# Optimization experiments

Measured on AMD Instinct MI355X. Metric: run time of the kernel, lower is better.

Reference implementation:

```python
import jax, jax.numpy as jnp
import numpy as np

NUM_SAMPLES = 1024


def _cdist(a, b):
    # a, b: (n, 3) -> (n, n) pairwise euclidean distances (torch.cdist p=2)
    d2 = jnp.sum((a[:, None, :] - b[None, :, :]) ** 2, axis=-1)
    return jnp.sqrt(jnp.maximum(d2, 0.0))


def _greedy_match_cost(cost):
    # Greedy sequential matching: repeatedly take the global argmin over
    # still-unmatched rows/cols, accumulate its cost, eliminate row+col.
    n = cost.shape[0]

    def step(carry, _):
        row_mask, col_mask, loss = carry
        valid = row_mask[:, None] & col_mask[None, :]
        masked = jnp.where(valid, cost, jnp.inf)
        idx = jnp.argmin(masked)  # row-major first-min == torch's min(dim=1)+argmin tiebreak
        r = idx // n
        c = idx % n
        loss = loss + cost[r, c]
        return (row_mask.at[r].set(False), col_mask.at[c].set(False), loss), None

    init = (jnp.ones((n,), dtype=bool), jnp.ones((n,), dtype=bool), jnp.float32(0.0))
    (_, _, loss), _ = jax.lax.scan(step, init, None, length=n)
    return loss / n


def setup_inputs() -> dict:
    key = jax.random.key(0)
    k1, k2, k3 = jax.random.split(key, 3)
    B, N, n = 8, 4096, NUM_SAMPLES
    S1 = jax.random.normal(k1, (B, N, 3), dtype=jnp.float32)
    S2 = jax.random.normal(k2, (B, N, 3), dtype=jnp.float32)
    # torch.randperm(N)[:n] per batch element: without-replacement sampling
    perm_keys = jax.random.split(k3, B)
    indices = jax.vmap(lambda k: jax.random.permutation(k, N)[:n])(perm_keys).astype(jnp.int32)
    return {"S1": S1, "S2": S2, "indices": indices}


def reference(S1, S2, indices):
    # sample the same indices from both sets, per batch (matches original loop)
    s1 = jnp.take_along_axis(S1, indices[:, :, None], axis=1)  # (B, n, 3)
    s2 = jnp.take_along_axis(S2, indices[:, :, None], axis=1)  # (B, n, 3)
    cost = jax.vmap(_cdist)(s1, s2)  # (B, n, n)
    losses = jax.vmap(_greedy_match_cost)(cost)  # (B,)
    return jnp.mean(losses)
```

## Files before the change

kernel.cpp:

```cpp
#include <hip/hip_runtime.h>
#include <stdint.h>

#define BATCH 8
#define NPTS 4096
#define NS 1024
#define KD 6

typedef unsigned long long u64;
typedef unsigned int u32;
typedef unsigned short u16;
typedef unsigned char u8;

#define DEADV (~0ull)
#define QNANB 0x7FC00000u
#define INFB  0x7F800000u

__device__ __forceinline__ float pdist3(float ax, float ay, float az,
                                        float bx, float by, float bz) {
    float dx = ax - bx, dy = ay - by, dz = az - bz;
    float d2 = __fmaf_rn(dz, dz, __fmaf_rn(dy, dy, dx * dx));
    return __fsqrt_rn(d2);
}

__device__ __forceinline__ u64 packv(float d, u32 row, u32 col) {
    return ((u64)__float_as_uint(d) << 20) | ((u64)row << 10) | (u64)col;
}

__device__ __forceinline__ u64 u64min2(u64 a, u64 b) { return a < b ? a : b; }

__device__ __forceinline__ u64 tree16(const u64* p) {
    u64 a0 = u64min2(p[0], p[1]),   a1 = u64min2(p[2], p[3]);
    u64 a2 = u64min2(p[4], p[5]),   a3 = u64min2(p[6], p[7]);
    u64 a4 = u64min2(p[8], p[9]),   a5 = u64min2(p[10], p[11]);
    u64 a6 = u64min2(p[12], p[13]), a7 = u64min2(p[14], p[15]);
    u64 b0 = u64min2(a0, a1), b1 = u64min2(a2, a3);
    u64 b2 = u64min2(a4, a5), b3 = u64min2(a6, a7);
    return u64min2(u64min2(b0, b1), u64min2(b2, b3));
}

template<int CTRL>
__device__ __forceinline__ u64 dpp_min_step(u64 m) {
    u32 lo = (u32)m, hi = (u32)(m >> 32);
    u32 olo = (u32)__builtin_amdgcn_update_dpp(-1, (int)lo, CTRL, 0xF, 0xF, false);
    u32 ohi = (u32)__builtin_amdgcn_update_dpp(-1, (int)hi, CTRL, 0xF, 0xF, false);
    u64 o = ((u64)ohi << 32) | olo;
    return o < m ? o : m;
}

__device__ __forceinline__ u64 wave_min_u64(u64 m) {
    m = dpp_min_step<0x111>(m);
    m = dpp_min_step<0x112>(m);
    m = dpp_min_step<0x114>(m);
    m = dpp_min_step<0x118>(m);
    m = dpp_min_step<0x142>(m);
    m = dpp_min_step<0x143>(m);
    u32 lo = (u32)__builtin_amdgcn_readlane((int)(u32)m, 63);
    u32 hi = (u32)__builtin_amdgcn_readlane((int)(u32)(m >> 32), 63);
    return ((u64)hi << 32) | lo;
}

__global__ void gather_k(const float* __restrict__ S1, const float* __restrict__ S2,
                         const int* __restrict__ idx,
                         float4* __restrict__ s1g, float4* __restrict__ s2g,
                         int* __restrict__ cnt) {
    int t = blockIdx.x * blockDim.x + threadIdx.x;
    if (t == 0) *cnt = 0;
    if (t >= BATCH * NS) return;
    int b = t >> 10;
    int j = idx[t];
    const float* p1 = S1 + ((size_t)b * NPTS + j) * 3;
    const float* p2 = S2 + ((size_t)b * NPTS + j) * 3;
    s1g[t] = make_float4(p1[0], p1[1], p1[2], 0.f);
    s2g[t] = make_float4(p2[0], p2[1], p2[2], 0.f);
}

__global__ void lists_k(const float4* __restrict__ s1g, const float4* __restrict__ s2g,
                        u64* __restrict__ rlist_g, u64* __restrict__ clist_g) {
    __shared__ float4 pts[NS];
    int gg = blockIdx.x * 4 + (threadIdx.x >> 6);
    int lane = threadIdx.x & 63;
    int side = (gg >= BATCH * NS) ? 1 : 0;
    int g = gg - side * (BATCH * NS);
    int b = g >> 10;
    u32 rc = (u32)(g & 1023);
    const float4* other = (side ? s1g : s2g) + (size_t)b * NS;
    for (int i = threadIdx.x; i < NS; i += 256) pts[i] = other[i];
    float4 a = side ? s2g[g] : s1g[g];
    __syncthreads();
    u64 cand[16];
    #pragma unroll
    for (int k = 0; k < 16; ++k) {
        int o = lane + (k << 6);
        float4 q = pts[o];
        float d = pdist3(a.x, a.y, a.z, q.x, q.y, q.z);
        cand[k] = side ? packv(d, (u32)o, rc) : packv(d, rc, (u32)o);
    }
    u64* out = (side ? clist_g : rlist_g) + (size_t)g * KD;
    for (int i = 0; i < KD; ++i) {
        u64 m1 = wave_min_u64(tree16(cand));
        if (lane == 0) out[i] = m1;
        #pragma unroll
        for (int k = 0; k < 16; ++k) cand[k] = (cand[k] == m1) ? DEADV : cand[k];
    }
}

__global__ void __launch_bounds__(1024, 1)
resolve_k(const float4* __restrict__ s1g, const float4* __restrict__ s2g,
          const u64* __restrict__ rlist_gl, const u64* __restrict__ clist_gl,
          float* __restrict__ loss_ws, int* __restrict__ cnt,
          float* __restrict__ out) {
    __shared__ u64 rlist[NS * KD];
    __shared__ u64 clist[NS * KD];
    __shared__ u64 rmin[NS];
    __shared__ u64 cmin[NS];
    __shared__ float4 s1c[NS];
    __shared__ float4 s2c[NS];
    __shared__ u16 pos1[NS], pos2[NS];
    __shared__ u32 am1[NS / 32], am2[NS / 32];
    __shared__ u8 rptrs[NS], cptrs[NS];
    __shared__ u16 qrow[NS], qcol[NS];
    __shared__ int wcntr[16], wcntc[16];
    __shared__ int qrn, qcn, matched, stale_n;
    float* lred = (float*)rlist;
    int b = blockIdx.x;
    int tid = threadIdx.x;
    int lane = tid & 63, wv = tid >> 6;

    {
        const float4* rs = (const float4*)(rlist_gl + (size_t)b * NS * KD);
        const float4* cs = (const float4*)(clist_gl + (size_t)b * NS * KD);
        float4* rd = (float4*)rlist;
        float4* cd = (float4*)clist;
        for (int i = tid; i < NS * KD / 2; i += 1024) { rd[i] = rs[i]; cd[i] = cs[i]; }
    }
    {
        float4 v1 = s1g[(size_t)b * NS + tid]; v1.w = __uint_as_float((u32)tid);
        s1c[tid] = v1;
        float4 v2 = s2g[(size_t)b * NS + tid]; v2.w = __uint_as_float((u32)tid);
        s2c[tid] = v2;
    }
    pos1[tid] = (u16)tid; pos2[tid] = (u16)tid;
    rptrs[tid] = 1; cptrs[tid] = 1;
    if (tid < NS / 32) { am1[tid] = ~0u; am2[tid] = ~0u; }
    if (tid == 0) { matched = 0; stale_n = NS; }
    __syncthreads();
    rmin[tid] = rlist[tid * KD];
    cmin[tid] = clist[tid * KD];
    float loss = 0.f;
    __syncthreads();

#define ALIVE1(i) ((am1[(u32)(i) >> 5] >> ((u32)(i) & 31u)) & 1u)
#define ALIVE2(i) ((am2[(u32)(i) >> 5] >> ((u32)(i) & 31u)) & 1u)

    for (int round = 0; round < NS; ++round) {
        u64 myk = rmin[tid];
        u32 c = (u32)myk & 1023u;
        bool mut = (myk != DEADV) && (cmin[c] == myk);
        __syncthreads();
        if (mut) {
            loss += __uint_as_float((u32)(myk >> 20));
            rmin[tid] = DEADV;
            cmin[c] = DEADV;
            atomicAnd(&am1[tid >> 5], ~(1u << (tid & 31)));
            atomicAnd(&am2[c >> 5],   ~(1u << (c & 31)));
            s1c[pos1[tid]].x = __uint_as_float(QNANB);
            s2c[pos2[c]].x   = __uint_as_float(QNANB);
        }
        u64 bal = __ballot((int)mut);
        if (lane == 0 && bal) atomicAdd(&matched, (int)__popcll(bal));
        if (tid == 0) { qrn = 0; qcn = 0; }
        __syncthreads();
        int m = matched;
        if (m >= NS) break;
        int live = NS - m;
        int stale = stale_n;
        bool rebuild = (stale * 4 > live * 5 + 64);
        u64 rk = rmin[tid];
        if (rk != DEADV) {
            if (!ALIVE2((u32)rk & 1023u)) {
                u32 p = rptrs[tid];
                bool found = false;
                while (p < KD) {
                    u64 e = rlist[tid * KD + p];
                    ++p;
                    if (e != DEADV && ALIVE2((u32)e & 1023u)) {
                        rmin[tid] = e; found = true; break;
                    }
                }
                rptrs[tid] = (u8)p;
                if (!found) { int s = atomicAdd(&qrn, 1); qrow[s] = (u16)tid; }
            }
        }
        u64 ck = cmin[tid];
        if (ck != DEADV) {
            if (!ALIVE1(((u32)ck >> 10) & 1023u)) {
                u32 p = cptrs[tid];
                bool found = false;
                while (p < KD) {
                    u64 e = clist[tid * KD + p];
                    ++p;
                    if (e != DEADV && ALIVE1(((u32)e >> 10) & 1023u)) {
                        cmin[tid] = e; found = true; break;
                    }
                }
                cptrs[tid] = (u8)p;
                if (!found) { int s = atomicAdd(&qcn, 1); qcol[s] = (u16)tid; }
            }
        }
        if (rebuild) {
            bool calive = ALIVE2(tid) != 0u;
            bool ralive = ALIVE1(tid) != 0u;
            float4 cv, rv;
            if (calive) cv = s2c[pos2[tid]];
            if (ralive) rv = s1c[pos1[tid]];
            u64 cb = __ballot((int)calive);
            u64 rb = __ballot((int)ralive);
            if (lane == 0) { wcntc[wv] = (int)__popcll(cb); wcntr[wv] = (int)__popcll(rb); }
            __syncthreads();
            int cbase = 0, rbase = 0;
            for (int j = 0; j < wv; ++j) { cbase += wcntc[j]; rbase += wcntr[j]; }
            int crank = (int)__popcll(cb & ((1ull << lane) - 1ull));
            int rrank = (int)__popcll(rb & ((1ull << lane) - 1ull));
            if (calive) { int np = cbase + crank; pos2[tid] = (u16)np; s2c[np] = cv; }
            if (ralive) { int np = rbase + rrank; pos1[tid] = (u16)np; s1c[np] = rv; }
        }
        __syncthreads();
        int nr = qrn, nc = qcn;
        int scan_n = rebuild ? live : stale;
        if (rebuild && tid == 0) stale_n = live;
        int tot = nr + nc;
        for (int qi = wv; qi < tot; qi += 16) {
            if (qi < nr) {
                u32 r = qrow[qi];
                float4 a = s1c[pos1[r]];
                float a1d = __uint_as_float(INFB), a2d = a1d;
                u32 a1i = 1023u, a2i = 1023u;
                #pragma unroll 4
                for (int i = lane; i < scan_n; i += 64) {
                    float4 q = s2c[i];
                    float d = pdist3(a.x, a.y, a.z, q.x, q.y, q.z);
                    u32 ci = __float_as_uint(q.w);
                    bool c1 = d < a1d;
                    bool c2 = d < a2d;
                    float td = c2 ? d : a2d;  u32 ti = c2 ? ci : a2i;
                    a2d = c1 ? a1d : td;      a2i = c1 ? a1i : ti;
                    a1d = c1 ? d : a1d;       a1i = c1 ? ci : a1i;
                }
                u32 b1 = __float_as_uint(a1d), b2 = __float_as_uint(a2d);
                u64 m1 = (b1 == INFB) ? DEADV : (((u64)b1 << 10) | a1i);
                u64 m2 = (b2 == INFB) ? DEADV : (((u64)b2 << 10) | a2i);
                u64 M1 = wave_min_u64(m1);
                u64 ck2 = (m1 == M1) ? m2 : m1;
                u64 M2 = wave_min_u64(ck2);
                if (lane == 0) {
                    u64 F1 = ((M1 >> 10) << 20) | ((u64)r << 10) | (M1 & 1023u);
                    u64 F2 = (M2 == DEADV) ? DEADV
                           : (((M2 >> 10) << 20) | ((u64)r << 10) | (M2 & 1023u));
                    rmin[r] = F1;
                    rlist[r * KD + KD - 1] = F2;
                    rptrs[r] = KD - 1;
                }
            } else {
                u32 cc = qcol[qi - nr];
                float4 a = s2c[pos2[cc]];
                float a1d = __uint_as_float(INFB), a2d = a1d;
                u32 a1i = 1023u, a2i = 1023u;
                #pragma unroll 4
                for (int i = lane; i < scan_n; i += 64) {
                    float4 q = s1c[i];
                    float d = pdist3(q.x, q.y, q.z, a.x, a.y, a.z);
                    u32 ri = __float_as_uint(q.w);
                    bool c1 = d < a1d;
                    bool c2 = d < a2d;
                    float td = c2 ? d : a2d;  u32 ti = c2 ? ri : a2i;
                    a2d = c1 ? a1d : td;      a2i = c1 ? a1i : ti;
                    a1d = c1 ? d : a1d;       a1i = c1 ? ri : a1i;
                }
                u32 b1 = __float_as_uint(a1d), b2 = __float_as_uint(a2d);
                u64 m1 = (b1 == INFB) ? DEADV : (((u64)b1 << 10) | a1i);
                u64 m2 = (b2 == INFB) ? DEADV : (((u64)b2 << 10) | a2i);
                u64 M1 = wave_min_u64(m1);
                u64 ck2 = (m1 == M1) ? m2 : m1;
                u64 M2 = wave_min_u64(ck2);
                if (lane == 0) {
                    u64 F1 = ((M1 >> 10) << 20) | ((M1 & 1023u) << 10) | (u64)cc;
                    u64 F2 = (M2 == DEADV) ? DEADV
                           : (((M2 >> 10) << 20) | ((M2 & 1023u) << 10) | (u64)cc);
                    cmin[cc] = F1;
                    clist[cc * KD + KD - 1] = F2;
                    cptrs[cc] = KD - 1;
                }
            }
        }
        __syncthreads();
    }

    lred[tid] = loss;
    __syncthreads();
    #pragma unroll
    for (int s = 512; s > 0; s >>= 1) {
        if (tid < s) lred[tid] += lred[tid + s];
        __syncthreads();
    }
    if (tid == 0) {
        atomicExch(&loss_ws[b], lred[0] * (1.0f / NS));
        __threadfence();
        int old = atomicAdd(cnt, 1);
        if (old == BATCH - 1) {
            __threadfence();
            float s = 0.f;
            for (int i = 0; i < BATCH; ++i) s += atomicAdd(&loss_ws[i], 0.0f);
            out[0] = s * (1.0f / BATCH);
        }
    }
}

extern "C" void kernel_launch(void* const* d_in, const int* in_sizes, int n_in,
                              void* d_out, int out_size, void* d_ws, size_t ws_size,
                              hipStream_t stream) {
    const float* S1 = (const float*)d_in[0];
    const float* S2 = (const float*)d_in[1];
    const int* idx  = (const int*)d_in[2];
    char* ws = (char*)d_ws;
    size_t o = 0;
    float4* s1g    = (float4*)(ws + o); o += (size_t)BATCH * NS * 16;
    float4* s2g    = (float4*)(ws + o); o += (size_t)BATCH * NS * 16;
    u64* rlist_g   = (u64*)(ws + o);    o += (size_t)BATCH * NS * KD * 8;
    u64* clist_g   = (u64*)(ws + o);    o += (size_t)BATCH * NS * KD * 8;
    float* loss_ws = (float*)(ws + o);  o += (size_t)BATCH * 4;
    int* cnt       = (int*)(ws + o);

    gather_k<<<(BATCH * NS + 255) / 256, 256, 0, stream>>>(S1, S2, idx, s1g, s2g, cnt);
    lists_k<<<2 * BATCH * NS / 4, 256, 0, stream>>>(s1g, s2g, rlist_g, clist_g);
    resolve_k<<<BATCH, 1024, 0, stream>>>(s1g, s2g, rlist_g, clist_g, loss_ws, cnt,
                                          (float*)d_out);
}
```

Before: 205.7 us.

## Finish last 64 live pairs in a single-wave register-resident matching tail

Once 64 or fewer rows and columns remain unmatched, the block-wide round loop exits. Survivors are compacted into small shared arrays, and one wavefront finishes the greedy mutual-min matching using DPP reductions, ds_bpermute and ballots. This replaces the many tail rounds that each needed block-wide __syncthreads with wave-local steps. The cost is extra code complexity, and results must still match the tie-breaking on the packed keys.

```diff
diff --git a/kernel.cpp b/kernel.cpp
--- a/kernel.cpp
+++ b/kernel.cpp
@@ -57,6 +57,30 @@
     u32 lo = (u32)__builtin_amdgcn_readlane((int)(u32)m, 63);
     u32 hi = (u32)__builtin_amdgcn_readlane((int)(u32)(m >> 32), 63);
     return ((u64)hi << 32) | lo;
+}
+
+template<int CTRL>
+__device__ __forceinline__ u64 dpp_or_step(u64 m) {
+    u32 lo = (u32)m, hi = (u32)(m >> 32);
+    u32 olo = (u32)__builtin_amdgcn_update_dpp(0, (int)lo, CTRL, 0xF, 0xF, false);
+    u32 ohi = (u32)__builtin_amdgcn_update_dpp(0, (int)hi, CTRL, 0xF, 0xF, false);
+    return m | (((u64)ohi << 32) | olo);
+}
+
+__device__ __forceinline__ u64 wave_or_u64(u64 m) {
+    m = dpp_or_step<0x111>(m);
+    m = dpp_or_step<0x112>(m);
+    m = dpp_or_step<0x114>(m);
+    m = dpp_or_step<0x118>(m);
+    m = dpp_or_step<0x142>(m);
+    m = dpp_or_step<0x143>(m);
+    u32 lo = (u32)__builtin_amdgcn_readlane((int)(u32)m, 63);
+    u32 hi = (u32)__builtin_amdgcn_readlane((int)(u32)(m >> 32), 63);
+    return ((u64)hi << 32) | lo;
+}
+
+__device__ __forceinline__ float readlane_f(float v, int l) {
+    return __uint_as_float((u32)__builtin_amdgcn_readlane((int)__float_as_uint(v), l));
 }
 
 __global__ void gather_k(const float* __restrict__ S1, const float* __restrict__ S2,
@@ -115,6 +139,7 @@
     __shared__ u64 cmin[NS];
     __shared__ float4 s1c[NS];
     __shared__ float4 s2c[NS];
+    __shared__ float4 e1c[64], e2c[64];
     __shared__ u16 pos1[NS], pos2[NS];
     __shared__ u32 am1[NS / 32], am2[NS / 32];
     __shared__ u8 rptrs[NS], cptrs[NS];
@@ -152,6 +177,7 @@
 #define ALIVE1(i) ((am1[(u32)(i) >> 5] >> ((u32)(i) & 31u)) & 1u)
 #define ALIVE2(i) ((am2[(u32)(i) >> 5] >> ((u32)(i) & 31u)) & 1u)
 
+    int elive = 0;
     for (int round = 0; round < NS; ++round) {
         u64 myk = rmin[tid];
         u32 c = (u32)myk & 1023u;
@@ -173,6 +199,7 @@
         int m = matched;
         if (m >= NS) break;
         int live = NS - m;
+        if (live <= 64) { elive = live; break; }
         int stale = stale_n;
         bool rebuild = (stale * 4 > live * 5 + 64);
         u64 rk = rmin[tid];
@@ -295,8 +322,91 @@
         __syncthreads();
     }
 
+    if (elive > 0) {
+        bool ralive = ALIVE1(tid) != 0u;
+        bool calive = ALIVE2(tid) != 0u;
+        u64 rb = __ballot((int)ralive);
+        u64 cb = __ballot((int)calive);
+        if (lane == 0) { wcntr[wv] = (int)__popcll(rb); wcntc[wv] = (int)__popcll(cb); }
+        __syncthreads();
+        int rbase = 0, cbase = 0;
+        for (int j = 0; j < wv; ++j) { rbase += wcntr[j]; cbase += wcntc[j]; }
+        int rrank = (int)__popcll(rb & ((1ull << lane) - 1ull));
+        int crank = (int)__popcll(cb & ((1ull << lane) - 1ull));
+        if (ralive) { int np = rbase + rrank; qrow[np] = (u16)tid; e1c[np] = s1c[pos1[tid]]; }
+        if (calive) { int np = cbase + crank; qcol[np] = (u16)tid; e2c[np] = s2c[pos2[tid]]; }
+    }
+    __syncthreads();
     lred[tid] = loss;
     __syncthreads();
+
+    if (elive > 0 && wv == 0) {
+        int j = lane;
+        bool aliveR = j < elive, aliveC = j < elive;
+        float4 rp = e1c[j];
+        float4 cp = e2c[j];
+        u32 rorig = (u32)qrow[j], corig = (u32)qcol[j];
+        u64 rmk = DEADV, cmk = DEADV;
+        u32 rmp = 0, cmp_ = 0;
+        for (int k = 0; k < elive; ++k) {
+            float4 ckp = e2c[k]; u32 cko = (u32)qcol[k];
+            float dr = pdist3(rp.x, rp.y, rp.z, ckp.x, ckp.y, ckp.z);
+            u64 kr = ((u64)__float_as_uint(dr) << 20) | ((u64)rorig << 10) | cko;
+            if (aliveR && kr < rmk) { rmk = kr; rmp = (u32)k; }
+            float4 rkp = e1c[k]; u32 rko = (u32)qrow[k];
+            float dc = pdist3(rkp.x, rkp.y, rkp.z, cp.x, cp.y, cp.z);
+            u64 kc = ((u64)__float_as_uint(dc) << 20) | ((u64)rko << 10) | corig;
+            if (aliveC && kc < cmk) { cmk = kc; cmp_ = (u32)k; }
+        }
+        float eloss = 0.f;
+        bool ematched = false;
+        while (__ballot((int)aliveR) != 0ull) {
+            int addr = (int)(rmp << 2);
+            u32 pl = (u32)__builtin_amdgcn_ds_bpermute(addr, (int)(u32)cmk);
+            u32 ph = (u32)__builtin_amdgcn_ds_bpermute(addr, (int)(u32)(cmk >> 32));
+            u64 cmin_at = ((u64)ph << 32) | pl;
+            bool mut = aliveR && (cmin_at == rmk);
+            u64 mutmask = __ballot((int)mut);
+            u64 ckill = wave_or_u64(mut ? (1ull << rmp) : 0ull);
+            if (mut) { eloss = __uint_as_float((u32)(rmk >> 20)); ematched = true; aliveR = false; }
+            if ((ckill >> j) & 1ull) aliveC = false;
+            bool rrep = aliveR && ((ckill >> rmp) & 1ull);
+            bool crep = aliveC && ((mutmask >> cmp_) & 1ull);
+            u64 rrm = __ballot((int)rrep);
+            while (rrm) {
+                int jr = (int)(__ffsll((long long)rrm) - 1); rrm &= rrm - 1ull;
+                float rx = readlane_f(rp.x, jr), ry = readlane_f(rp.y, jr), rz = readlane_f(rp.z, jr);
+                u32 ro = (u32)__builtin_amdgcn_readlane((int)rorig, jr);
+                u64 kk = DEADV;
+                if (aliveC) {
+                    float d = pdist3(rx, ry, rz, cp.x, cp.y, cp.z);
+                    kk = ((u64)__float_as_uint(d) << 20) | ((u64)ro << 10) | corig;
+                }
+                u64 M = wave_min_u64(kk);
+                u64 eq = __ballot((int)(kk == M));
+                u32 np = (u32)(__ffsll((long long)eq) - 1);
+                if (j == jr) { rmk = M; rmp = np; }
+            }
+            u64 crm = __ballot((int)crep);
+            while (crm) {
+                int jc = (int)(__ffsll((long long)crm) - 1); crm &= crm - 1ull;
+                float cx = readlane_f(cp.x, jc), cy = readlane_f(cp.y, jc), cz = readlane_f(cp.z, jc);
+                u32 co = (u32)__builtin_amdgcn_readlane((int)corig, jc);
+                u64 kk = DEADV;
+                if (aliveR) {
+                    float d = pdist3(rp.x, rp.y, rp.z, cx, cy, cz);
+                    kk = ((u64)__float_as_uint(d) << 20) | ((u64)rorig << 10) | co;
+                }
+                u64 M = wave_min_u64(kk);
+                u64 eq = __ballot((int)(kk == M));
+                u32 np = (u32)(__ffsll((long long)eq) - 1);
+                if (j == jc) { cmk = M; cmp_ = np; }
+            }
+        }
+        if (ematched) lred[rorig] += eloss;
+    }
+    __syncthreads();
+
     #pragma unroll
     for (int s = 512; s > 0; s >>= 1) {
         if (tid < s) lred[tid] += lred[tid + s];
```

New measurement: 279.1 us. +35.6%, slower.
